# Kernel optimization log

Measured on AMD Instinct MI355X. Metric: run time of the kernel, lower is better.

Reference implementation:

```python
import jax, jax.numpy as jnp
import numpy as np

NUM_HEADS = 16

def setup_inputs() -> dict:
    key = jax.random.key(0)
    ks = jax.random.split(key, 7)
    B, S, D = 2, 2048, 1024
    X = jax.random.normal(ks[0], (B, S, D), dtype=jnp.float32)
    s = 1.0 / np.sqrt(D)
    Wq = jax.random.normal(ks[1], (D, D), dtype=jnp.float32) * s
    Wk = jax.random.normal(ks[2], (D, D), dtype=jnp.float32) * s
    Wv = jax.random.normal(ks[3], (D, D), dtype=jnp.float32) * s
    Wo = jax.random.normal(ks[4], (D, D), dtype=jnp.float32) * s
    bo = jnp.zeros((D,), dtype=jnp.float32)
    return {"X": X, "Wq": Wq, "Wk": Wk, "Wv": Wv, "Wo": Wo, "bo": bo}

def reference(X, Wq, Wk, Wv, Wo, bo):
    B, S, D = X.shape
    H = NUM_HEADS
    hd = D // H
    # project and split heads -> [B, H, S, hd]
    def split(t):
        return t.reshape(B, S, H, hd).transpose(0, 2, 1, 3)
    q = split(X @ Wq)
    k = split(X @ Wk)
    v = split(X @ Wv)
    scores = jnp.einsum('bhqd,bhkd->bhqk', q, k) / jnp.sqrt(jnp.float32(hd))
    causal = jnp.tril(jnp.ones((S, S), dtype=bool))
    scores = jnp.where(causal, scores, -jnp.inf)
    weights = jax.nn.softmax(scores, axis=-1)  # dropout p=0 -> identity
    ctx = jnp.einsum('bhqk,bhkd->bhqd', weights, v)
    ctx = ctx.transpose(0, 2, 1, 3).reshape(B, S, D)
    return ctx @ Wo + bo
```

## Files before the change

kernel.cpp:

```cpp
#include <hip/hip_runtime.h>


typedef __attribute__((ext_vector_type(8))) short short8;
typedef __attribute__((ext_vector_type(4))) float floatx4;

__device__ inline unsigned short f2bf(float f) {
  unsigned u = __float_as_uint(f);
  unsigned r = (u + 0x7fffu + ((u >> 16) & 1u)) >> 16;
  return (unsigned short)r;
}

__device__ __forceinline__ float fast_exp2(float x) {
#if __has_builtin(__builtin_amdgcn_exp2f)
  return __builtin_amdgcn_exp2f(x);
#else
  float r;
  asm volatile("v_exp_f32_e32 %0, %1" : "=v"(r) : "v"(x));
  return r;
#endif
}

__device__ __forceinline__ void gll16(const unsigned short* g, unsigned short* l) {
  __builtin_amdgcn_global_load_lds(
      (const __attribute__((address_space(1))) unsigned int*)(g),
      (__attribute__((address_space(3))) unsigned int*)(l),
      16, 0, 0);
}

constexpr int B_ = 2, S_ = 2048, D_ = 1024, H_ = 16, HD_ = 64;

__global__ __launch_bounds__(256) void prep_inputs(
    const float* __restrict__ x, unsigned short* __restrict__ xb,
    const float* __restrict__ w0, const float* __restrict__ w1,
    const float* __restrict__ w2, const float* __restrict__ w3,
    unsigned short* __restrict__ wt_base)
{
  if (blockIdx.z == 4) {
    const int tid = threadIdx.y * 32 + threadIdx.x;
    const size_t base =
        ((size_t)(blockIdx.y * 32 + blockIdx.x) * 256 + tid) * 16;
#pragma unroll
    for (int half = 0; half < 2; ++half) {
      const size_t i = base + half * 8;
      float4 a = *(const float4*)(x + i);
      float4 b = *(const float4*)(x + i + 4);
      short8 o;
      o[0] = (short)f2bf(a.x); o[1] = (short)f2bf(a.y);
      o[2] = (short)f2bf(a.z); o[3] = (short)f2bf(a.w);
      o[4] = (short)f2bf(b.x); o[5] = (short)f2bf(b.y);
      o[6] = (short)f2bf(b.z); o[7] = (short)f2bf(b.w);
      *(short8*)(xb + i) = o;
    }
    return;
  }
  const float* src;
  switch (blockIdx.z) {
    case 0: src = w0; break;
    case 1: src = w1; break;
    case 2: src = w2; break;
    default: src = w3; break;
  }
  unsigned short* dst = wt_base + (size_t)blockIdx.z * 1024 * 1024;
  __shared__ unsigned short t[32][33];
  const int bx = blockIdx.x * 32;
  const int by = blockIdx.y * 32;
  const int x_ = threadIdx.x;
  for (int yy = threadIdx.y; yy < 32; yy += 8)
    t[yy][x_] = f2bf(src[(size_t)(by + yy) * 1024 + bx + x_]);
  __syncthreads();
  for (int yy = threadIdx.y; yy < 32; yy += 8)
    dst[(size_t)(bx + yy) * 1024 + by + x_] = t[x_][yy];
}

__global__ __launch_bounds__(256) void transpose_v(
    const unsigned short* __restrict__ Vb, unsigned short* __restrict__ Vt)
{
  __shared__ unsigned short t[32][33];
  const int bh = blockIdx.z;
  const int b = bh >> 4, h = bh & 15;
  const int s0 = blockIdx.x * 32, d0 = blockIdx.y * 32;
  const int x = threadIdx.x;
  for (int yy = threadIdx.y; yy < 32; yy += 8)
    t[yy][x] = Vb[(size_t)(b * 2048 + s0 + yy) * 1024 + h * 64 + d0 + x];
  __syncthreads();
  for (int yy = threadIdx.y; yy < 32; yy += 8)
    Vt[((size_t)bh * 64 + d0 + yy) * 2048 + s0 + x] = t[x][yy];
}

__global__ __launch_bounds__(256) void gemm256_qkv(
    const unsigned short* __restrict__ A,
    const unsigned short* __restrict__ Bt,
    unsigned short* __restrict__ Qo,
    unsigned short* __restrict__ Ko,
    unsigned short* __restrict__ Vo)
{
  __shared__ unsigned short sA[2][128 * 32];
  __shared__ unsigned short sB[2][128 * 32];
  const int K = 1024;
  const int m0 = blockIdx.y * 128;
  const int bn0 = blockIdx.x * 128;

  const int tid = threadIdx.x, wave = tid >> 6, lane = tid & 63;
  const int g = lane >> 4, ml = lane & 15;
  const int wm = wave & 1, wn = wave >> 1;

  const unsigned short* ag0 = A + (size_t)(m0 + (tid >> 2)) * K + (tid & 3) * 8;
  const unsigned short* ag1 = ag0 + (size_t)64 * K;
  const unsigned short* bg0 = Bt + (size_t)(bn0 + (tid >> 2)) * K + (tid & 3) * 8;
  const unsigned short* bg1 = bg0 + (size_t)64 * K;
  const int woff = wave * 512;

  floatx4 acc[4][4];
#pragma unroll
  for (int mt = 0; mt < 4; ++mt)
#pragma unroll
    for (int nt = 0; nt < 4; ++nt) acc[mt][nt] = (floatx4){0.f, 0.f, 0.f, 0.f};

  for (int k0 = 0; k0 < K; k0 += 64) {
    __syncthreads();
#pragma unroll
    for (int t = 0; t < 2; ++t) {
      gll16(ag0 + k0 + t * 32, sA[t] + woff);
      gll16(ag1 + k0 + t * 32, sA[t] + 2048 + woff);
      gll16(bg0 + k0 + t * 32, sB[t] + woff);
      gll16(bg1 + k0 + t * 32, sB[t] + 2048 + woff);
    }
    __syncthreads();
#pragma unroll
    for (int t = 0; t < 2; ++t) {
      short8 af[4], bf[4];
#pragma unroll
      for (int mt = 0; mt < 4; ++mt)
        af[mt] = *(const short8*)(sA[t] + (wm * 64 + mt * 16 + ml) * 32 + g * 8);
#pragma unroll
      for (int nt = 0; nt < 4; ++nt)
        bf[nt] = *(const short8*)(sB[t] + (wn * 64 + nt * 16 + ml) * 32 + g * 8);
#pragma unroll
      for (int mt = 0; mt < 4; ++mt)
#pragma unroll
        for (int nt = 0; nt < 4; ++nt)
          acc[mt][nt] = __builtin_amdgcn_mfma_f32_16x16x32_bf16(
              af[mt], bf[nt], acc[mt][nt], 0, 0, 0);
    }
  }

  const int proj = blockIdx.x >> 3;
  unsigned short* out = (proj == 0) ? Qo : (proj == 1) ? Ko : Vo;
  const int col0 = (blockIdx.x & 7) * 128;
#pragma unroll
  for (int mt = 0; mt < 4; ++mt) {
#pragma unroll
    for (int nt = 0; nt < 4; ++nt) {
      const int col = col0 + wn * 64 + nt * 16 + ml;
#pragma unroll
      for (int r = 0; r < 4; ++r) {
        const int row = m0 + wm * 64 + mt * 16 + g * 4 + r;
        out[(size_t)row * 1024 + col] = f2bf(acc[mt][nt][r]);
      }
    }
  }
}

__global__ __launch_bounds__(256) void gemm_wo64(
    const unsigned short* __restrict__ A,
    const unsigned short* __restrict__ Bt,
    const float* __restrict__ bias,
    float* __restrict__ C)
{
  __shared__ unsigned short sA[4][64 * 32];
  __shared__ unsigned short sB[4][128 * 32];
  const int K = 1024;
  const int m0 = blockIdx.y * 64;
  const int bn0 = blockIdx.x * 128;
  const int tid = threadIdx.x, wave = tid >> 6, lane = tid & 63;
  const int g = lane >> 4, ml = lane & 15;
  const int wm = wave & 1, wn = wave >> 1;

  const unsigned short* ag =
      A + (size_t)(m0 + wave * 16 + (lane >> 2)) * K + (lane & 3) * 8;
  const unsigned short* bg0 = Bt + (size_t)(bn0 + (tid >> 2)) * K + (tid & 3) * 8;
  const unsigned short* bg1 = bg0 + (size_t)64 * K;
  const int woff = wave * 512;

  floatx4 acc[2][4];
#pragma unroll
  for (int mt = 0; mt < 2; ++mt)
#pragma unroll
    for (int nt = 0; nt < 4; ++nt) acc[mt][nt] = (floatx4){0.f, 0.f, 0.f, 0.f};

  for (int k0 = 0; k0 < K; k0 += 128) {
    __syncthreads();
#pragma unroll
    for (int t = 0; t < 4; ++t) {
      gll16(ag + k0 + t * 32, sA[t] + woff);
      gll16(bg0 + k0 + t * 32, sB[t] + woff);
      gll16(bg1 + k0 + t * 32, sB[t] + 2048 + woff);
    }
    __syncthreads();
#pragma unroll
    for (int t = 0; t < 4; ++t) {
      short8 af[2], bf[4];
#pragma unroll
      for (int mt = 0; mt < 2; ++mt)
        af[mt] = *(const short8*)(sA[t] + (wm * 32 + mt * 16 + ml) * 32 + g * 8);
#pragma unroll
      for (int nt = 0; nt < 4; ++nt)
        bf[nt] = *(const short8*)(sB[t] + (wn * 64 + nt * 16 + ml) * 32 + g * 8);
#pragma unroll
      for (int mt = 0; mt < 2; ++mt)
#pragma unroll
        for (int nt = 0; nt < 4; ++nt)
          acc[mt][nt] = __builtin_amdgcn_mfma_f32_16x16x32_bf16(
              af[mt], bf[nt], acc[mt][nt], 0, 0, 0);
    }
  }

#pragma unroll
  for (int mt = 0; mt < 2; ++mt) {
#pragma unroll
    for (int nt = 0; nt < 4; ++nt) {
      const int col = bn0 + wn * 64 + nt * 16 + ml;
      const float badd = bias[col];
#pragma unroll
      for (int r = 0; r < 4; ++r) {
        const int row = m0 + wm * 32 + mt * 16 + g * 4 + r;
        C[(size_t)row * 1024 + col] = acc[mt][nt][r] + badd;
      }
    }
  }
}

constexpr int KTPB = 2;

struct AttnLds {
  unsigned short k0[KTPB][64 * 32];
  unsigned short k1[KTPB][64 * 32];
  unsigned short v0[KTPB][64 * 32];
  unsigned short v1[KTPB][64 * 32];
};
union __align__(16) AttnLdsU {
  AttnLds t;
  float comb[4 * 64 * 36];
};

__device__ __forceinline__ void attn_tile(
    const short8* aq,
    const unsigned short* sK0, const unsigned short* sK1,
    const unsigned short* sV0, const unsigned short* sV1,
    floatx4* acc, float& l,
    const bool diag, const int qg , const int kb ,
    const int g, const int ml)
{
  const float C1 = 0.18033688f;
  const float C2 = -34.6246810f;

  floatx4 s[4];
#pragma unroll
  for (int nb = 0; nb < 4; ++nb) {
    s[nb] = (floatx4){0.f, 0.f, 0.f, 0.f};
    short8 bk0 = *(const short8*)(sK0 + (nb * 16 + ml) * 32 + g * 8);
    s[nb] = __builtin_amdgcn_mfma_f32_16x16x32_bf16(bk0, aq[0], s[nb], 0, 0, 0);
    short8 bk1 = *(const short8*)(sK1 + (nb * 16 + ml) * 32 + g * 8);
    s[nb] = __builtin_amdgcn_mfma_f32_16x16x32_bf16(bk1, aq[1], s[nb], 0, 0, 0);
  }

  unsigned wb[4][4];
#pragma unroll
  for (int nb = 0; nb < 4; ++nb) {
#pragma unroll
    for (int r = 0; r < 4; ++r) {
      float wv = fast_exp2(fmaf(s[nb][r], C1, C2));
      if (diag && (kb + nb * 16 + r > qg)) wv = 0.f;
      const unsigned bits = __float_as_uint(wv) & 0xffff0000u;
      wb[nb][r] = bits;
      l += __uint_as_float(bits);
    }
  }

  unsigned pk[4][2];
#pragma unroll
  for (int nb = 0; nb < 4; ++nb) {
    pk[nb][0] = __builtin_amdgcn_perm(wb[nb][1], wb[nb][0], 0x07060302u);
    pk[nb][1] = __builtin_amdgcn_perm(wb[nb][3], wb[nb][2], 0x07060302u);
  }

  unsigned Fr[2][4];
#pragma unroll
  for (int rr = 0; rr < 2; ++rr) {
    unsigned a0 = pk[0][rr], a1 = pk[1][rr];
    unsigned a2 = pk[2][rr], a3 = pk[3][rr];
    asm("v_permlane32_swap_b32 %0, %1" : "+v"(a0), "+v"(a1));
    asm("v_permlane32_swap_b32 %0, %1" : "+v"(a2), "+v"(a3));
    asm("v_permlane16_swap_b32 %0, %1" : "+v"(a0), "+v"(a1));
    asm("v_permlane16_swap_b32 %0, %1" : "+v"(a2), "+v"(a3));
    Fr[0][rr] = a0; Fr[0][2 + rr] = a1;
    Fr[1][rr] = a2; Fr[1][2 + rr] = a3;
  }

#pragma unroll
  for (int f = 0; f < 2; ++f) {
    union { unsigned u[4]; short8 s8; } uap;
    uap.u[0] = Fr[f][0]; uap.u[1] = Fr[f][1];
    uap.u[2] = Fr[f][2]; uap.u[3] = Fr[f][3];
    const short8 ap = uap.s8;
    const unsigned short* sv = f ? sV1 : sV0;
#pragma unroll
    for (int jd = 0; jd < 4; ++jd) {
      short8 bv = *(const short8*)(sv + (jd * 16 + ml) * 32 + g * 8);
      acc[jd] = __builtin_amdgcn_mfma_f32_16x16x32_bf16(ap, bv, acc[jd], 0, 0, 0);
    }
  }
}

__global__ __launch_bounds__(512) void attn_v12(
    const unsigned short* __restrict__ Q,
    const unsigned short* __restrict__ Kg,
    const unsigned short* __restrict__ Vt,
    unsigned short* __restrict__ CTX)
{
  __shared__ AttnLdsU lds;

  const int bh = blockIdx.y;
  const int b = bh >> 4, h = bh & 15;
  const int p = blockIdx.x;
  const int qbA = p, qbB = 31 - p;
  const int qA0 = qbA * 64, qB0 = qbB * 64;
  const int tid = threadIdx.x, w = tid >> 6, lane = tid & 63;
  const int slice = w & 3, par = w >> 2;
  const int g = lane >> 4, ml = lane & 15;

  const size_t headoff = (size_t)b * S_ * D_ + (size_t)h * HD_;
  const size_t vtoff   = (size_t)bh * HD_ * S_;

  short8 aqA[2], aqB[2];
  {
    const unsigned short* qp =
        Q + headoff + (size_t)(qA0 + slice * 16 + ml) * D_ + g * 8;
    aqA[0] = *(const short8*)qp;
    aqA[1] = *(const short8*)(qp + 32);
  }
  {
    const unsigned short* qp =
        Q + headoff + (size_t)(qB0 + slice * 16 + ml) * D_ + g * 8;
    aqB[0] = *(const short8*)qp;
    aqB[1] = *(const short8*)(qp + 32);
  }

  floatx4 accA[4], accB[4];
#pragma unroll
  for (int jd = 0; jd < 4; ++jd) {
    accA[jd] = (floatx4){0.f, 0.f, 0.f, 0.f};
    accB[jd] = (floatx4){0.f, 0.f, 0.f, 0.f};
  }
  float lA = 0.f, lB = 0.f;
  const int qgA = qA0 + slice * 16 + ml;
  const int qgB = qB0 + slice * 16 + ml;

  const int sw = slice;
  const unsigned short* kgb =
      Kg + headoff + (size_t)(sw * 16 + (lane >> 2)) * D_ + (lane & 3) * 8;
  const unsigned short* vgb =
      Vt + vtoff + (size_t)(sw * 16 + (lane >> 2)) * S_ + (lane & 3) * 8;
  const int woff = sw * 512;

  const int ntiles = qbB + 1;
  for (int kt0 = 0; kt0 < ntiles; kt0 += KTPB) {
    const int cnt = (ntiles - kt0 < KTPB) ? (ntiles - kt0) : KTPB;
    __syncthreads();
#pragma unroll
    for (int t = 0; t < KTPB; ++t) {
      if (t >= cnt) break;
      const int kt = kt0 + t;
      if (w < 4) {
        const size_t ko = (size_t)kt * 64 * D_;
        gll16(kgb + ko,      lds.t.k0[t] + woff);
        gll16(kgb + ko + 32, lds.t.k1[t] + woff);
      } else {
        gll16(vgb + kt * 64,      lds.t.v0[t] + woff);
        gll16(vgb + kt * 64 + 32, lds.t.v1[t] + woff);
      }
    }
    __syncthreads();

    if (par < cnt) {
      const int kt = kt0 + par;
      const int kb = kt * 64 + g * 4;
      attn_tile(aqB, lds.t.k0[par], lds.t.k1[par], lds.t.v0[par], lds.t.v1[par],
                accB, lB, kt == qbB, qgB, kb, g, ml);
      if (kt <= qbA)
        attn_tile(aqA, lds.t.k0[par], lds.t.k1[par], lds.t.v0[par], lds.t.v1[par],
                  accA, lA, kt == qbA, qgA, kb, g, ml);
    }
  }

  __syncthreads();
  {
    float* slot = lds.comb + (size_t)(slice * 64 + lane) * 36;
    if (par == 1) {
#pragma unroll
      for (int jd = 0; jd < 4; ++jd) {
        *(floatx4*)(slot + jd * 4) = accA[jd];
        *(floatx4*)(slot + 16 + jd * 4) = accB[jd];
      }
      slot[32] = lA;
      slot[33] = lB;
    }
    __syncthreads();
    if (par == 1) return;
#pragma unroll
    for (int jd = 0; jd < 4; ++jd) {
      accA[jd] += *(const floatx4*)(slot + jd * 4);
      accB[jd] += *(const floatx4*)(slot + 16 + jd * 4);
    }
    lA += slot[32];
    lB += slot[33];
  }

  lA += __shfl_xor(lA, 16); lA += __shfl_xor(lA, 32);
  lB += __shfl_xor(lB, 16); lB += __shfl_xor(lB, 32);
  const float liA = 1.0f / lA;
  const float liB = 1.0f / lB;
  float lrA[4], lrB[4];
#pragma unroll
  for (int r = 0; r < 4; ++r) {
    lrA[r] = __shfl(liA, g * 4 + r);
    lrB[r] = __shfl(liB, g * 4 + r);
  }

#pragma unroll
  for (int r = 0; r < 4; ++r) {
    const int rowA = qA0 + slice * 16 + g * 4 + r;
    const int rowB = qB0 + slice * 16 + g * 4 + r;
#pragma unroll
    for (int jd = 0; jd < 4; ++jd) {
      CTX[headoff + (size_t)rowA * D_ + jd * 16 + ml] = f2bf(accA[jd][r] * lrA[r]);
      CTX[headoff + (size_t)rowB * D_ + jd * 16 + ml] = f2bf(accB[jd][r] * lrB[r]);
    }
  }
}

extern "C" void kernel_launch(void* const* d_in, const int* in_sizes, int n_in,
                              void* d_out, int out_size, void* d_ws, size_t ws_size,
                              hipStream_t stream)
{
  const float* X  = (const float*)d_in[0];
  const float* Wq = (const float*)d_in[1];
  const float* Wk = (const float*)d_in[2];
  const float* Wv = (const float*)d_in[3];
  const float* Wo = (const float*)d_in[4];
  const float* bo = (const float*)d_in[5];

  char* ws = (char*)d_ws;
  const size_t MB = 1024 * 1024;

  unsigned short* Qb  = (unsigned short*)(ws);
  unsigned short* Kb  = (unsigned short*)(ws + 8 * MB);
  unsigned short* Xb  = (unsigned short*)(ws + 16 * MB);
  unsigned short* WT  = (unsigned short*)(ws + 24 * MB);
  unsigned short* WoT = WT + (size_t)3 * 1024 * 1024;
  unsigned short* Vb  = (unsigned short*)d_out;
  unsigned short* Vt  = Xb;

  prep_inputs<<<dim3(32, 32, 5), dim3(32, 8), 0, stream>>>(
      X, Xb, Wq, Wk, Wv, Wo, WT);
  gemm256_qkv<<<dim3(24, 32), 256, 0, stream>>>(Xb, WT, Qb, Kb, Vb);
  transpose_v<<<dim3(64, 2, 32), dim3(32, 8), 0, stream>>>(Vb, Vt);
  attn_v12<<<dim3(16, B_ * H_), 512, 0, stream>>>(Qb, Kb, Vt, Qb);
  gemm_wo64<<<dim3(8, 64), 256, 0, stream>>>(Qb, WoT, bo, (float*)d_out);
}
```

Measured before the change: 201.1 us.

## Double-buffer attention K/V tiles in LDS and swizzle blocks across XCDs

The attention kernel now prefetches the next pair of K/V tiles into a second LDS buffer while the current pair is being processed, leaving one barrier per iteration instead of two. The aim is to hide global-to-LDS load latency behind the MFMA work. The launch also becomes a 1D grid whose block index is remapped so that the 8 interleaved block groups each get contiguous batch-head work, which should improve L2 reuse of K/V per XCD. The cost is twice the LDS footprint for the tile buffers, which may reduce occupancy.

```diff
diff --git a/kernel.cpp b/kernel.cpp
--- a/kernel.cpp
+++ b/kernel.cpp
@@ -233,10 +233,10 @@
 constexpr int KTPB = 2;
 
 struct AttnLds {
-  unsigned short k0[KTPB][64 * 32];
-  unsigned short k1[KTPB][64 * 32];
-  unsigned short v0[KTPB][64 * 32];
-  unsigned short v1[KTPB][64 * 32];
+  unsigned short k0[2][KTPB][64 * 32];
+  unsigned short k1[2][KTPB][64 * 32];
+  unsigned short v0[2][KTPB][64 * 32];
+  unsigned short v1[2][KTPB][64 * 32];
 };
 union __align__(16) AttnLdsU {
   AttnLds t;
@@ -312,7 +312,7 @@
   }
 }
 
-__global__ __launch_bounds__(512) void attn_v12(
+__global__ __launch_bounds__(512) void attn_v13(
     const unsigned short* __restrict__ Q,
     const unsigned short* __restrict__ Kg,
     const unsigned short* __restrict__ Vt,
@@ -320,9 +320,12 @@
 {
   __shared__ AttnLdsU lds;
 
-  const int bh = blockIdx.y;
+  const int L = blockIdx.x;
+  const int rid = (L & 7) * 64 + (L >> 3);
+  const int p = rid & 15;
+  const int bh = rid >> 4;
+
   const int b = bh >> 4, h = bh & 15;
-  const int p = blockIdx.x;
   const int qbA = p, qbB = 31 - p;
   const int qA0 = qbA * 64, qB0 = qbB * 64;
   const int tid = threadIdx.x, w = tid >> 6, lane = tid & 63;
@@ -364,36 +367,59 @@
   const int woff = sw * 512;
 
   const int ntiles = qbB + 1;
-  for (int kt0 = 0; kt0 < ntiles; kt0 += KTPB) {
-    const int cnt = (ntiles - kt0 < KTPB) ? (ntiles - kt0) : KTPB;
-    __syncthreads();
+
+  {
+    const int cnt = (ntiles < KTPB) ? ntiles : KTPB;
 #pragma unroll
     for (int t = 0; t < KTPB; ++t) {
       if (t >= cnt) break;
-      const int kt = kt0 + t;
       if (w < 4) {
-        const size_t ko = (size_t)kt * 64 * D_;
-        gll16(kgb + ko,      lds.t.k0[t] + woff);
-        gll16(kgb + ko + 32, lds.t.k1[t] + woff);
+        const size_t ko = (size_t)t * 64 * D_;
+        gll16(kgb + ko,      lds.t.k0[0][t] + woff);
+        gll16(kgb + ko + 32, lds.t.k1[0][t] + woff);
       } else {
-        gll16(vgb + kt * 64,      lds.t.v0[t] + woff);
-        gll16(vgb + kt * 64 + 32, lds.t.v1[t] + woff);
+        gll16(vgb + t * 64,      lds.t.v0[0][t] + woff);
+        gll16(vgb + t * 64 + 32, lds.t.v1[0][t] + woff);
       }
     }
-    __syncthreads();
-
+  }
+  __syncthreads();
+
+  for (int kt0 = 0; kt0 < ntiles; kt0 += KTPB) {
+    const int bufi = (kt0 >> 1) & 1;
+    const int nxt = kt0 + KTPB;
+    if (nxt < ntiles) {
+      const int cn = (ntiles - nxt < KTPB) ? (ntiles - nxt) : KTPB;
+#pragma unroll
+      for (int t = 0; t < KTPB; ++t) {
+        if (t >= cn) break;
+        const int kt = nxt + t;
+        if (w < 4) {
+          const size_t ko = (size_t)kt * 64 * D_;
+          gll16(kgb + ko,      lds.t.k0[bufi ^ 1][t] + woff);
+          gll16(kgb + ko + 32, lds.t.k1[bufi ^ 1][t] + woff);
+        } else {
+          gll16(vgb + kt * 64,      lds.t.v0[bufi ^ 1][t] + woff);
+          gll16(vgb + kt * 64 + 32, lds.t.v1[bufi ^ 1][t] + woff);
+        }
+      }
+    }
+
+    const int cnt = (ntiles - kt0 < KTPB) ? (ntiles - kt0) : KTPB;
     if (par < cnt) {
       const int kt = kt0 + par;
       const int kb = kt * 64 + g * 4;
-      attn_tile(aqB, lds.t.k0[par], lds.t.k1[par], lds.t.v0[par], lds.t.v1[par],
+      attn_tile(aqB, lds.t.k0[bufi][par], lds.t.k1[bufi][par],
+                lds.t.v0[bufi][par], lds.t.v1[bufi][par],
                 accB, lB, kt == qbB, qgB, kb, g, ml);
       if (kt <= qbA)
-        attn_tile(aqA, lds.t.k0[par], lds.t.k1[par], lds.t.v0[par], lds.t.v1[par],
+        attn_tile(aqA, lds.t.k0[bufi][par], lds.t.k1[bufi][par],
+                  lds.t.v0[bufi][par], lds.t.v1[bufi][par],
                   accA, lA, kt == qbA, qgA, kb, g, ml);
     }
-  }
-
-  __syncthreads();
+    __syncthreads();
+  }
+
   {
     float* slot = lds.comb + (size_t)(slice * 64 + lane) * 36;
     if (par == 1) {
@@ -465,6 +491,6 @@
       X, Xb, Wq, Wk, Wv, Wo, WT);
   gemm256_qkv<<<dim3(24, 32), 256, 0, stream>>>(Xb, WT, Qb, Kb, Vb);
   transpose_v<<<dim3(64, 2, 32), dim3(32, 8), 0, stream>>>(Vb, Vt);
-  attn_v12<<<dim3(16, B_ * H_), 512, 0, stream>>>(Qb, Kb, Vt, Qb);
+  attn_v13<<<dim3(512), 512, 0, stream>>>(Qb, Kb, Vt, Qb);
   gemm_wo64<<<dim3(8, 64), 256, 0, stream>>>(Qb, WoT, bo, (float*)d_out);
 }
```

Result: faster. 187.8 us (-6.6%).
